# Optimization experiments

Measured on AMD Instinct MI355X. Metric: run time of the kernel, lower is better.

The kernel has to match this reference:

```python
import jax, jax.numpy as jnp
import numpy as np

VOCAB = 32000
D_IN = 1024      # == 2 * N_OUT so highway uses raw x (k=3 SRU path)
N_OUT = 512      # hidden per direction
N_LAYERS = 4
L, B = 1024, 16


def _sru_bidir_layer(x, W, b, n):
    """x: (L,B,2n), W: (2n, 6n) [dir0: xt,f,r | dir1: xt,f,r], b: (4n,) = [bf(2n), br(2n)]."""
    u = jnp.einsum('lbd,dk->lbk', x, W)  # (L,B,6n)
    bf, br = b[:2 * n], b[2 * n:]
    hs, cs = [], []
    for d, rev in ((0, False), (1, True)):
        ud = u[..., d * 3 * n:(d + 1) * 3 * n]
        xt = ud[..., :n]
        f = jax.nn.sigmoid(ud[..., n:2 * n] + bf[d * n:(d + 1) * n])
        r = jax.nn.sigmoid(ud[..., 2 * n:3 * n] + br[d * n:(d + 1) * n])
        xp = x[..., d * n:(d + 1) * n]  # highway input (k=3 case)

        def step(c, inp):
            xt_t, f_t, r_t, xp_t = inp
            c = f_t * c + (1.0 - f_t) * xt_t
            h = r_t * jnp.tanh(c) + (1.0 - r_t) * xp_t
            return c, h

        c0 = jnp.zeros((x.shape[1], n), x.dtype)
        c_last, h = jax.lax.scan(step, c0, (xt, f, r, xp), reverse=rev)
        hs.append(h)
        cs.append(c_last)
    return jnp.concatenate(hs, -1), jnp.concatenate(cs, -1)


def setup_inputs() -> dict:
    key = jax.random.key(0)
    k1, k2, k3, k4 = jax.random.split(key, 4)
    rnn_input = jax.random.randint(k1, (L, B), 0, VOCAB, dtype=jnp.int32)
    input_lengths = jax.random.randint(k2, (B,), 1, L + 1, dtype=jnp.int32)
    emb = jax.random.normal(k3, (VOCAB, D_IN), dtype=jnp.float32) * 0.05
    scale = 1.0 / np.sqrt(D_IN)
    Ws = jax.random.normal(k4, (N_LAYERS, D_IN, 6 * N_OUT), dtype=jnp.float32) * scale
    bs = jnp.zeros((N_LAYERS, 4 * N_OUT), dtype=jnp.float32)
    return {"rnn_input": rnn_input, "input_lengths": input_lengths,
            "emb": emb, "Ws": Ws, "bs": bs}


def reference(rnn_input, input_lengths, emb, Ws, bs):
    # input_lengths is unused in the original forward (no packing applied to SRU input)
    n = Ws.shape[-1] // 6
    x = emb[rnn_input]  # (L,B,D_IN)
    c_finals = []
    for l in range(Ws.shape[0]):
        x, c = _sru_bidir_layer(x, Ws[l], bs[l], n)
        c_finals.append(c)
    hidden = jnp.stack(c_finals, 0)  # (N_LAYERS, B, 2n)
    return x, hidden
```

## Files before the change

### kernel.cpp

```cpp
#include <hip/hip_runtime.h>
#include <hip/hip_bf16.h>
#include <cmath>

#define L_SEQ  1024
#define BATCH  16
#define NOUT   512
#define DIN    1024
#define NBIG   3072
#define NLAYERS 4
#define NTOK   (L_SEQ * BATCH)
#define NCHAIN 16384
#define SEG    32
#define SEGLEN (L_SEQ / SEG)

typedef __attribute__((ext_vector_type(8))) short bf16x8;
typedef __attribute__((ext_vector_type(4))) float f32x4;

__device__ __forceinline__ unsigned short f2bf(float f) {
    unsigned x = __float_as_uint(f);
    unsigned r = (x + 0x7fffu + ((x >> 16) & 1u)) >> 16;
    return (unsigned short)r;
}
__device__ __forceinline__ float bf2f(unsigned short hv) {
    return __uint_as_float((unsigned)hv << 16);
}
__device__ __forceinline__ float sigmf(float v) {
    return 1.f / (1.f + __expf(-v));
}
__device__ __forceinline__ void async16(const void* g, const void* l) {
    __builtin_amdgcn_global_load_lds(
        (const __attribute__((address_space(1))) unsigned int*)g,
        (__attribute__((address_space(3))) unsigned int*)l, 16, 0, 0);
}

__global__ __launch_bounds__(256)
void transpose_w(const float* __restrict__ Ws, unsigned short* __restrict__ Wt) {
    __shared__ float tile[32][33];
    int l = blockIdx.z;
    const float* W = Ws + (size_t)l * DIN * NBIG;
    unsigned short* Wo = Wt + (size_t)l * NBIG * DIN;
    int n0 = blockIdx.x * 32, k0 = blockIdx.y * 32;
    int tx = threadIdx.x & 31, ty = threadIdx.x >> 5;
    #pragma unroll
    for (int i = 0; i < 4; i++)
        tile[ty + 8 * i][tx] = W[(size_t)(k0 + ty + 8 * i) * NBIG + n0 + tx];
    __syncthreads();
    #pragma unroll
    for (int i = 0; i < 4; i++)
        Wo[(size_t)(n0 + ty + 8 * i) * DIN + k0 + tx] = f2bf(tile[tx][ty + 8 * i]);
}

__global__ void embed_kernel(const int* __restrict__ tok,
                             const float* __restrict__ emb,
                             float* __restrict__ x,
                             unsigned short* __restrict__ xbf) {
    int t = blockIdx.x;
    int row = tok[t];
    float4 v = ((const float4*)(emb + (size_t)row * DIN))[threadIdx.x];
    ((float4*)(x + (size_t)t * DIN))[threadIdx.x] = v;
    ushort4 h;
    h.x = f2bf(v.x); h.y = f2bf(v.y); h.z = f2bf(v.z); h.w = f2bf(v.w);
    ((ushort4*)(xbf + (size_t)t * DIN))[threadIdx.x] = h;
}

__global__ __launch_bounds__(256)
void gemm_bf16(const unsigned short* __restrict__ Abf,
               const unsigned short* __restrict__ Bt,
               unsigned short* __restrict__ u_xt,
               unsigned short* __restrict__ u_f,
               unsigned short* __restrict__ u_r) {
    __shared__ __align__(16) unsigned short As[128 * 64];
    __shared__ __align__(16) unsigned short Bs[128 * 64];

    const int tid  = threadIdx.x;
    const int lane = tid & 63;
    const int w    = tid >> 6;
    const int wm   = w & 1, wn = w >> 1;
    const int quad = lane >> 4, l16 = lane & 15;

    const int M0 = blockIdx.y * 128;
    const int N0 = blockIdx.x * 128;

    f32x4 acc[4][4];
    #pragma unroll
    for (int i = 0; i < 4; i++)
        #pragma unroll
        for (int j = 0; j < 4; j++)
            acc[i][j] = (f32x4){0.f, 0.f, 0.f, 0.f};

    const int sr = lane >> 3;
    const int sc = (lane & 7) ^ sr;

    for (int k0 = 0; k0 < DIN; k0 += 64) {
        #pragma unroll
        for (int g = 0; g < 4; g++) {
            int rbase = w * 32 + g * 8;
            int r = rbase + sr;
            async16(Abf + (size_t)(M0 + r) * DIN + k0 + sc * 8, &As[rbase * 64]);
            async16(Bt  + (size_t)(N0 + r) * DIN + k0 + sc * 8, &Bs[rbase * 64]);
        }
        __syncthreads();

        #pragma unroll
        for (int s = 0; s < 2; s++) {
            bf16x8 af[4], bg[4];
            #pragma unroll
            for (int t = 0; t < 4; t++) {
                int ra = wm * 64 + t * 16 + l16;
                int sa = (s * 4 + quad) ^ (ra & 7);
                af[t] = *(const bf16x8*)&As[ra * 64 + sa * 8];
                int rb = wn * 64 + t * 16 + l16;
                int sb = (s * 4 + quad) ^ (rb & 7);
                bg[t] = *(const bf16x8*)&Bs[rb * 64 + sb * 8];
            }
            #pragma unroll
            for (int i = 0; i < 4; i++)
                #pragma unroll
                for (int j = 0; j < 4; j++)
                    acc[i][j] = __builtin_amdgcn_mfma_f32_16x16x32_bf16(af[i], bg[j], acc[i][j], 0, 0, 0);
        }
        __syncthreads();
    }

    #pragma unroll
    for (int i = 0; i < 4; i++) {
        int gm = M0 + wm * 64 + i * 16 + quad * 4;
        #pragma unroll
        for (int j = 0; j < 4; j++) {
            int gn = N0 + wn * 64 + j * 16 + l16;
            int dir  = gn >= 3 * NOUT;
            int jj   = gn - dir * 3 * NOUT;
            int plane = jj >> 9;
            int feat  = jj & 511;
            unsigned short* p = (plane == 0 ? u_xt : plane == 1 ? u_f : u_r)
                                + (size_t)gm * DIN + dir * NOUT + feat;
            #pragma unroll
            for (int r = 0; r < 4; r++) p[(size_t)r * DIN] = f2bf(acc[i][j][r]);
        }
    }
}


__global__ __launch_bounds__(256)
void scan_phaseA(const unsigned short* __restrict__ u_xt, const unsigned short* __restrict__ u_f,
                 const float* __restrict__ bias,
                 float* __restrict__ Aseg, float* __restrict__ Bseg) {
    int g = blockIdx.x * 256 + threadIdx.x;
    int chain = g & (NCHAIN - 1);
    int s = g >> 14;
    int rest = chain & 1023;
    float bf = bias[rest];

    int d = rest >> 9;
    int t0 = d ? (L_SEQ - 1 - s * SEGLEN) : (s * SEGLEN);
    int sgn = d ? -1 : 1;
    long long idx = (long long)t0 * NCHAIN + chain;
    long long step = (long long)sgn * NCHAIN;

    float c = 0.f, A = 1.f;
    #pragma unroll 8
    for (int j = 0; j < SEGLEN; j++) {
        float xt = bf2f(u_xt[idx]);
        float f = sigmf(bf2f(u_f[idx]) + bf);
        c = f * c + (1.f - f) * xt;
        A *= f;
        idx += step;
    }
    Aseg[g] = A;
    Bseg[g] = c;
}

__global__ __launch_bounds__(256)
void scan_phaseB(const float* __restrict__ Aseg, const float* __restrict__ Bseg,
                 float* __restrict__ cstart, float* __restrict__ c_out) {
    int chain = blockIdx.x * 256 + threadIdx.x;
    float c = 0.f;
    #pragma unroll
    for (int s = 0; s < SEG; s++) {
        int g = s * NCHAIN + chain;
        cstart[g] = c;
        c = Aseg[g] * c + Bseg[g];
    }
    c_out[chain] = c;
}

__global__ __launch_bounds__(256)
void scan_phaseC(const unsigned short* __restrict__ u_xt, const unsigned short* __restrict__ u_f,
                 const unsigned short* __restrict__ u_r,
                 float* __restrict__ x, unsigned short* __restrict__ xbf,
                 const float* __restrict__ bias, const float* __restrict__ cstart,
                 int write_bf) {
    int g = blockIdx.x * 256 + threadIdx.x;
    int chain = g & (NCHAIN - 1);
    int s = g >> 14;
    int rest = chain & 1023;
    float bf = bias[rest];
    float br = bias[1024 + rest];

    int d = rest >> 9;
    int t0 = d ? (L_SEQ - 1 - s * SEGLEN) : (s * SEGLEN);
    int sgn = d ? -1 : 1;
    long long idx = (long long)t0 * NCHAIN + chain;
    long long step = (long long)sgn * NCHAIN;

    float c = cstart[g];
    #pragma unroll 4
    for (int j = 0; j < SEGLEN; j++) {
        float xt = bf2f(u_xt[idx]);
        float f = sigmf(bf2f(u_f[idx]) + bf);
        float r = sigmf(bf2f(u_r[idx]) + br);
        float xp = x[idx];
        c = f * c + (1.f - f) * xt;
        float th = 1.f - 2.f / (__expf(2.f * c) + 1.f);
        float h = r * th + (1.f - r) * xp;
        x[idx] = h;
        if (write_bf) xbf[idx] = f2bf(h);
        idx += step;
    }
}

extern "C" void kernel_launch(void* const* d_in, const int* in_sizes, int n_in,
                              void* d_out, int out_size, void* d_ws, size_t ws_size,
                              hipStream_t stream) {
    const int*   tok = (const int*)d_in[0];
    const float* emb = (const float*)d_in[2];
    const float* Ws  = (const float*)d_in[3];
    const float* bs  = (const float*)d_in[4];

    float* out    = (float*)d_out;
    float* x      = out;
    float* hidden = out + (size_t)NTOK * DIN;

    char* ws = (char*)d_ws;
    unsigned short* u_xt   = (unsigned short*)ws;
    unsigned short* u_f    = (unsigned short*)(ws + (32u  << 20));
    unsigned short* u_r    = (unsigned short*)(ws + (64u  << 20));
    unsigned short* xbf    = (unsigned short*)(ws + (96u  << 20));
    unsigned short* Wt     = (unsigned short*)(ws + (128u << 20));
    float*          Aseg   = (float*)(ws + (152u << 20));
    float*          Bseg   = (float*)(ws + (154u << 20));
    float*          cstart = (float*)(ws + (156u << 20));

    transpose_w<<<dim3(NBIG / 32, DIN / 32, NLAYERS), 256, 0, stream>>>(Ws, Wt);
    embed_kernel<<<NTOK, 256, 0, stream>>>(tok, emb, x, xbf);

    const int scan_blocks = NCHAIN * SEG / 256;

    for (int l = 0; l < NLAYERS; l++) {
        const unsigned short* Wl = Wt + (size_t)l * NBIG * DIN;
        const float* b = bs + (size_t)l * 4 * NOUT;
        gemm_bf16<<<dim3(NBIG / 128, NTOK / 128), 256, 0, stream>>>(xbf, Wl, u_xt, u_f, u_r);
        scan_phaseA<<<scan_blocks, 256, 0, stream>>>(u_xt, u_f, b, Aseg, Bseg);
        scan_phaseB<<<NCHAIN / 256, 256, 0, stream>>>(Aseg, Bseg, cstart,
                                                      hidden + (size_t)l * BATCH * DIN);
        scan_phaseC<<<scan_blocks, 256, 0, stream>>>(u_xt, u_f, u_r, x, xbf, b, cstart,
                                                     l < NLAYERS - 1);
    }
}
```

Measured before the change: 980.5 us.

## Rewrite GEMM as 256x256 tile, 8-wave, double-buffered pipelined kernel

Replaces the 128x128, 4-wave GEMM with a 256x256 tile run by 8 waves. LDS is double-buffered and split into half-tiles, so async global-to-LDS loads for the next k-slice overlap with MFMA work on the current one, coordinated by explicit waitcnt and barriers. The kernel also raises MFMA priority with setprio and swizzles block order for L2 locality. In exchange it uses 128KB of LDS and more accumulator registers, and the hand-tuned waitcnt sequencing is fragile.

Measured after the change: 923.2 us. -5.9%, faster.

```diff
diff --git a/kernel.cpp b/kernel.cpp
--- a/kernel.cpp
+++ b/kernel.cpp
@@ -63,27 +63,102 @@
     ((ushort4*)(xbf + (size_t)t * DIN))[threadIdx.x] = h;
 }
 
-__global__ __launch_bounds__(256)
+
+#define STAGE_A(b, mh, kt, src)                                             \
+    do {                                                                    \
+        _Pragma("unroll")                                                   \
+        for (int q = 0; q < 2; q++) {                                       \
+            int rbase = q * 128 + (mh) * 64 + w * 8;                        \
+            async16((src) + (size_t)(rbase + sr) * DIN + (kt) * 64 + sc * 8,\
+                    &lds[b][0][rbase * 64]);                                \
+        }                                                                   \
+    } while (0)
+
+#define STAGE_B(b, nh, kt, src)                                             \
+    do {                                                                    \
+        _Pragma("unroll")                                                   \
+        for (int q = 0; q < 2; q++) {                                       \
+            int gi = q * 8 + w;                                             \
+            int rbase = (gi >> 2) * 64 + (nh) * 32 + (gi & 3) * 8;          \
+            async16((src) + (size_t)(rbase + sr) * DIN + (kt) * 64 + sc * 8,\
+                    &lds[b][1][rbase * 64]);                                \
+        }                                                                   \
+    } while (0)
+
+#define LOAD_A(b, mh)                                                       \
+    do {                                                                    \
+        _Pragma("unroll")                                                   \
+        for (int i = 0; i < 4; i++) {                                       \
+            int ra = wm * 128 + (mh) * 64 + i * 16 + l16;                   \
+            _Pragma("unroll")                                               \
+            for (int kk = 0; kk < 2; kk++) {                                \
+                int slot = (kk * 4 + quad) ^ (ra & 7);                      \
+                af[i][kk] = *(const bf16x8*)&lds[b][0][ra * 64 + slot * 8]; \
+            }                                                               \
+        }                                                                   \
+    } while (0)
+
+#define LOAD_B(b, nh)                                                       \
+    do {                                                                    \
+        _Pragma("unroll")                                                   \
+        for (int j = 0; j < 2; j++) {                                       \
+            int rb = wn * 64 + (nh) * 32 + j * 16 + l16;                    \
+            _Pragma("unroll")                                               \
+            for (int kk = 0; kk < 2; kk++) {                                \
+                int slot = (kk * 4 + quad) ^ (rb & 7);                      \
+                bg[j][kk] = *(const bf16x8*)&lds[b][1][rb * 64 + slot * 8]; \
+            }                                                               \
+        }                                                                   \
+    } while (0)
+
+#define MMA(mh, nh)                                                         \
+    do {                                                                    \
+        __builtin_amdgcn_s_setprio(1);                                      \
+        _Pragma("unroll")                                                   \
+        for (int i = 0; i < 4; i++)                                         \
+            _Pragma("unroll")                                               \
+            for (int j = 0; j < 2; j++)                                     \
+                _Pragma("unroll")                                           \
+                for (int kk = 0; kk < 2; kk++)                              \
+                    acc[(mh) * 4 + i][(nh) * 2 + j] =                       \
+                        __builtin_amdgcn_mfma_f32_16x16x32_bf16(            \
+                            af[i][kk], bg[j][kk],                           \
+                            acc[(mh) * 4 + i][(nh) * 2 + j], 0, 0, 0);      \
+        __builtin_amdgcn_s_setprio(0);                                      \
+    } while (0)
+
+#define BAR()   __builtin_amdgcn_s_barrier()
+#define LGKM0() do { asm volatile("s_waitcnt lgkmcnt(0)" ::: "memory");     \
+                     __builtin_amdgcn_sched_barrier(0); } while (0)
+#define LGKM8() asm volatile("s_waitcnt lgkmcnt(8)" ::: "memory")
+#define VM6()   asm volatile("s_waitcnt vmcnt(6)" ::: "memory")
+#define VM0()   asm volatile("s_waitcnt vmcnt(0)" ::: "memory")
+
+__global__ __launch_bounds__(512)
 void gemm_bf16(const unsigned short* __restrict__ Abf,
                const unsigned short* __restrict__ Bt,
                unsigned short* __restrict__ u_xt,
                unsigned short* __restrict__ u_f,
                unsigned short* __restrict__ u_r) {
-    __shared__ __align__(16) unsigned short As[128 * 64];
-    __shared__ __align__(16) unsigned short Bs[128 * 64];
+    __shared__ __align__(16) unsigned short lds[2][2][256 * 64];
 
     const int tid  = threadIdx.x;
     const int lane = tid & 63;
     const int w    = tid >> 6;
-    const int wm   = w & 1, wn = w >> 1;
+    const int wm   = w >> 2, wn = w & 3;
     const int quad = lane >> 4, l16 = lane & 15;
 
-    const int M0 = blockIdx.y * 128;
-    const int N0 = blockIdx.x * 128;
-
-    f32x4 acc[4][4];
-    #pragma unroll
-    for (int i = 0; i < 4; i++)
+    const int flat = blockIdx.y * (NBIG / 256) + blockIdx.x;
+    const int swz  = (flat & 7) * (NTOK / 256 * NBIG / 256 / 8) + (flat >> 3);
+    const int M0 = (swz / (NBIG / 256)) * 256;
+    const int N0 = (swz % (NBIG / 256)) * 256;
+
+    const unsigned short* Asrc = Abf + (size_t)M0 * DIN;
+    const unsigned short* Bsrc = Bt  + (size_t)N0 * DIN;
+
+    f32x4 acc[8][4];
+    #pragma unroll
+    for (int i = 0; i < 8; i++)
         #pragma unroll
         for (int j = 0; j < 4; j++)
             acc[i][j] = (f32x4){0.f, 0.f, 0.f, 0.f};
@@ -91,40 +166,50 @@
     const int sr = lane >> 3;
     const int sc = (lane & 7) ^ sr;
 
-    for (int k0 = 0; k0 < DIN; k0 += 64) {
-        #pragma unroll
-        for (int g = 0; g < 4; g++) {
-            int rbase = w * 32 + g * 8;
-            int r = rbase + sr;
-            async16(Abf + (size_t)(M0 + r) * DIN + k0 + sc * 8, &As[rbase * 64]);
-            async16(Bt  + (size_t)(N0 + r) * DIN + k0 + sc * 8, &Bs[rbase * 64]);
-        }
-        __syncthreads();
-
-        #pragma unroll
-        for (int s = 0; s < 2; s++) {
-            bf16x8 af[4], bg[4];
-            #pragma unroll
-            for (int t = 0; t < 4; t++) {
-                int ra = wm * 64 + t * 16 + l16;
-                int sa = (s * 4 + quad) ^ (ra & 7);
-                af[t] = *(const bf16x8*)&As[ra * 64 + sa * 8];
-                int rb = wn * 64 + t * 16 + l16;
-                int sb = (s * 4 + quad) ^ (rb & 7);
-                bg[t] = *(const bf16x8*)&Bs[rb * 64 + sb * 8];
-            }
-            #pragma unroll
-            for (int i = 0; i < 4; i++)
-                #pragma unroll
-                for (int j = 0; j < 4; j++)
-                    acc[i][j] = __builtin_amdgcn_mfma_f32_16x16x32_bf16(af[i], bg[j], acc[i][j], 0, 0, 0);
-        }
-        __syncthreads();
-    }
-
-    #pragma unroll
-    for (int i = 0; i < 4; i++) {
-        int gm = M0 + wm * 64 + i * 16 + quad * 4;
+    bf16x8 af[4][2], bg[2][2];
+
+    STAGE_A(0, 0, 0, Asrc); STAGE_B(0, 0, 0, Bsrc);
+    STAGE_B(0, 1, 0, Bsrc); STAGE_A(0, 1, 0, Asrc);
+    STAGE_A(1, 0, 1, Asrc); STAGE_B(1, 1, 1, Bsrc); STAGE_A(1, 1, 1, Asrc);
+    VM6();
+    BAR();
+
+    const int NITER = DIN / 128;
+    for (int t = 0; t < NITER; t++) {
+        const int k1 = 2 * t + 1;
+        const bool more = (t < NITER - 1);
+
+        LOAD_A(0, 0); LOAD_B(0, 0);
+        STAGE_B(1, 0, k1, Bsrc);
+        LGKM8(); BAR(); LGKM0(); MMA(0, 0); BAR();
+        LOAD_B(0, 1);
+        if (more) STAGE_A(0, 0, k1 + 1, Asrc);
+        BAR(); LGKM0(); MMA(0, 1); BAR();
+        LOAD_A(0, 1);
+        if (more) STAGE_B(0, 1, k1 + 1, Bsrc);
+        BAR(); LGKM0(); MMA(1, 1); BAR();
+        LOAD_B(0, 0);
+        if (more) { STAGE_A(0, 1, k1 + 1, Asrc); VM6(); }
+        else      { VM0(); }
+        BAR(); LGKM0(); MMA(1, 0); BAR();
+
+        LOAD_A(1, 0); LOAD_B(1, 0);
+        if (more) STAGE_B(0, 0, k1 + 1, Bsrc);
+        LGKM8(); BAR(); LGKM0(); MMA(0, 0); BAR();
+        LOAD_B(1, 1);
+        if (more) STAGE_A(1, 0, k1 + 2, Asrc);
+        BAR(); LGKM0(); MMA(0, 1); BAR();
+        LOAD_A(1, 1);
+        if (more) STAGE_B(1, 1, k1 + 2, Bsrc);
+        BAR(); LGKM0(); MMA(1, 1); BAR();
+        LOAD_B(1, 0);
+        if (more) { STAGE_A(1, 1, k1 + 2, Asrc); VM6(); }
+        BAR(); LGKM0(); MMA(1, 0); BAR();
+    }
+
+    #pragma unroll
+    for (int i = 0; i < 8; i++) {
+        int gm = M0 + wm * 128 + i * 16 + quad * 4;
         #pragma unroll
         for (int j = 0; j < 4; j++) {
             int gn = N0 + wn * 64 + j * 16 + l16;
@@ -249,7 +334,7 @@
     for (int l = 0; l < NLAYERS; l++) {
         const unsigned short* Wl = Wt + (size_t)l * NBIG * DIN;
         const float* b = bs + (size_t)l * 4 * NOUT;
-        gemm_bf16<<<dim3(NBIG / 128, NTOK / 128), 256, 0, stream>>>(xbf, Wl, u_xt, u_f, u_r);
+        gemm_bf16<<<dim3(NBIG / 256, NTOK / 256), 512, 0, stream>>>(xbf, Wl, u_xt, u_f, u_r);
         scan_phaseA<<<scan_blocks, 256, 0, stream>>>(u_xt, u_f, b, Aseg, Bseg);
         scan_phaseB<<<NCHAIN / 256, 256, 0, stream>>>(Aseg, Bseg, cstart,
                                                       hidden + (size_t)l * BATCH * DIN);
```
